# Performance work log

Measured on AMD Instinct MI355X. Metric: run time of the kernel, lower is better.

Reference implementation:

```python
import jax, jax.numpy as jnp
import numpy as np

N, E = 50000, 800000
HID, HEADS, EDIM = 64, 4, 32
HC = HID * HEADS
NEG_SLOPE = 0.2
LN_EPS = 1e-5


def setup_inputs() -> dict:
    key = jax.random.key(0)
    ks = jax.random.split(key, 16)
    s = lambda d: 1.0 / np.sqrt(d)
    return {
        "x": jax.random.normal(ks[0], (N, HID), jnp.float32),
        "edge_index": jax.random.randint(ks[1], (2, E), 0, N, jnp.int64),
        "edge_attr": jax.random.normal(ks[2], (E, EDIM), jnp.float32),
        # GATv2Conv params
        "W_l": jax.random.normal(ks[3], (HID, HC), jnp.float32) * s(HID),
        "b_l": jnp.zeros((HC,), jnp.float32),
        "W_r": jax.random.normal(ks[4], (HID, HC), jnp.float32) * s(HID),
        "b_r": jnp.zeros((HC,), jnp.float32),
        "W_e": jax.random.normal(ks[5], (EDIM, HC), jnp.float32) * s(EDIM),
        "att": jax.random.normal(ks[6], (HEADS, HID), jnp.float32) * s(HID),
        "bias_gat": jnp.zeros((HC,), jnp.float32),
        # block params
        "W1": jax.random.normal(ks[7], (HID, HC), jnp.float32) * s(HID),
        "b1": jnp.zeros((HC,), jnp.float32),
        "gamma": jnp.ones((HC,), jnp.float32),
        "beta": jnp.zeros((HC,), jnp.float32),
        "W2": jax.random.normal(ks[8], (HC, HID), jnp.float32) * s(HC),
        "b2": jnp.zeros((HID,), jnp.float32),
    }


def _gatv2(x, edge_index, edge_attr, W_l, b_l, W_r, b_r, W_e, att, bias_gat):
    src, dst = edge_index[0], edge_index[1]
    x_l = (x @ W_l + b_l).reshape(N, HEADS, HID)  # source transform
    x_r = (x @ W_r + b_r).reshape(N, HEADS, HID)  # target transform
    e = (edge_attr @ W_e).reshape(E, HEADS, HID)
    m = x_l[src] + x_r[dst] + e                    # [E, H, C]
    m = jax.nn.leaky_relu(m, NEG_SLOPE)
    alpha = jnp.einsum('ehc,hc->eh', m, att)       # [E, H]
    # segment softmax over incoming edges of each target node
    amax = jax.ops.segment_max(alpha, dst, num_segments=N)
    alpha = jnp.exp(alpha - amax[dst])
    denom = jax.ops.segment_sum(alpha, dst, num_segments=N)
    alpha = alpha / (denom[dst] + 1e-16)
    out = jax.ops.segment_sum(x_l[src] * alpha[..., None], dst, num_segments=N)
    return out.reshape(N, HC) + bias_gat


def reference(x, edge_index, edge_attr, W_l, b_l, W_r, b_r, W_e, att, bias_gat,
              W1, b1, gamma, beta, W2, b2):
    h = _gatv2(x, edge_index, edge_attr, W_l, b_l, W_r, b_r, W_e, att, bias_gat)
    xl = jnp.tanh(x @ W1 + b1)
    z = xl + h
    mu = jnp.mean(z, axis=-1, keepdims=True)
    var = jnp.var(z, axis=-1, keepdims=True)
    z = (z - mu) * jax.lax.rsqrt(var + LN_EPS) * gamma + beta
    return jnp.tanh(z @ W2 + b2)
```

## Files before the change

kernel.cpp:

```cpp
#include <hip/hip_runtime.h>
#include <math.h>

#define N_NODES 50000
#define N_EDGES 800000
#define HID 64
#define HEADS 4
#define HC 256
#define NEG_SLOPE 0.2f
#define LN_EPS 1e-5f
#define EDGE_BLOCKS 2048

typedef __attribute__((ext_vector_type(8))) short bf16x8;
typedef __attribute__((ext_vector_type(8))) unsigned short u16x8;
typedef __attribute__((ext_vector_type(4))) float f32x4;

__device__ __forceinline__ float bf2f(unsigned short u) {
    return __uint_as_float(((unsigned int)u) << 16);
}
__device__ __forceinline__ unsigned short f2bf(float f) {
    unsigned int u = __float_as_uint(f);
    u = (u + 0x7fffu + ((u >> 16) & 1u)) >> 16;
    return (unsigned short)u;
}
__device__ __forceinline__ float fast_tanh(float v) {
    const float c = fminf(fmaxf(v, -15.f), 15.f);
    const float e = __expf(2.f * c);
    return 1.f - 2.f / (e + 1.f);
}

__global__ __launch_bounds__(256) void k_node_transform(
    const float* __restrict__ x,
    const float* __restrict__ W_l, const float* __restrict__ b_l,
    const float* __restrict__ W_r, const float* __restrict__ b_r,
    unsigned short* __restrict__ xl_t, unsigned short* __restrict__ xr_t)
{
    __shared__ float xs[16][64];
    __shared__ unsigned short tl[16][256], tr[16][256];
    const int n0 = blockIdx.x * 16;
    const int t = threadIdx.x;
    for (int i = t; i < 16 * 64; i += 256) xs[i >> 6][i & 63] = x[n0 * 64 + i];
    __syncthreads();

    float accl[16], accr[16];
    const float bl = b_l[t], br = b_r[t];
#pragma unroll
    for (int n = 0; n < 16; n++) { accl[n] = bl; accr[n] = br; }
    for (int k = 0; k < 64; k++) {
        const float wl = W_l[k * 256 + t];
        const float wr = W_r[k * 256 + t];
#pragma unroll
        for (int n = 0; n < 16; n++) {
            accl[n] = fmaf(xs[n][k], wl, accl[n]);
            accr[n] = fmaf(xs[n][k], wr, accr[n]);
        }
    }
    const int pos = (t & 15) * 16 + (t >> 4);
#pragma unroll
    for (int n = 0; n < 16; n++) {
        tl[n][pos] = f2bf(accl[n]);
        tr[n][pos] = f2bf(accr[n]);
    }
    __syncthreads();
    const int n = t >> 4, q = t & 15;
#pragma unroll
    for (int i = 0; i < 4; i++) {
        *(ushort4*)(xl_t + (size_t)(n0 + n) * 256 + q * 16 + i * 4) = *(const ushort4*)&tl[n][q * 16 + i * 4];
        *(ushort4*)(xr_t + (size_t)(n0 + n) * 256 + q * 16 + i * 4) = *(const ushort4*)&tr[n][q * 16 + i * 4];
    }
}

__global__ __launch_bounds__(256) void k_prep(
    const float* __restrict__ W_e, const float* __restrict__ att,
    unsigned short* __restrict__ wfrag, unsigned short* __restrict__ att_t)
{
    const int t = threadIdx.x;
#pragma unroll
    for (int s = 0; s < 4; s++) {
        const int slot = t * 4 + s;
        const int nt = slot >> 6, ls = slot & 63;
        const int col = nt * 16 + (ls & 15);
        const int kb = (ls >> 4) * 8;
#pragma unroll
        for (int j = 0; j < 8; j++)
            wfrag[slot * 8 + j] = f2bf(W_e[(kb + j) * 256 + col]);
    }
    att_t[t] = f2bf(att[(t & 15) * 16 + (t >> 4)]);
}

__global__ __launch_bounds__(256) void k_hist(const int* __restrict__ ei, int* __restrict__ count)
{
    const int e = blockIdx.x * 256 + threadIdx.x;
    if (e < N_EDGES) atomicAdd(&count[ei[N_EDGES + e]], 1);
}

__global__ __launch_bounds__(1024) void k_scan(const int* __restrict__ count, int* __restrict__ off)
{
    __shared__ int wsum[16];
    __shared__ int s_carry;
    const int t = threadIdx.x, lane = t & 63, wv = t >> 6;
    if (t == 0) s_carry = 0;
    __syncthreads();
    for (int base = 0; base < N_NODES; base += 8192) {
        const int idx0 = base + t * 8;
        int v[8];
#pragma unroll
        for (int j = 0; j < 8; j++) { int i = idx0 + j; v[j] = (i < N_NODES) ? count[i] : 0; }
#pragma unroll
        for (int j = 1; j < 8; j++) v[j] += v[j - 1];
        const int tot = v[7];
        int sc = tot;
#pragma unroll
        for (int s = 1; s < 64; s <<= 1) { int o = __shfl_up(sc, s, 64); if (lane >= s) sc += o; }
        if (lane == 63) wsum[wv] = sc;
        __syncthreads();
        const int carry = s_carry;
        int woff = 0;
        for (int u = 0; u < wv; u++) woff += wsum[u];
        const int ebase = carry + woff + (sc - tot);
#pragma unroll
        for (int j = 0; j < 8; j++) {
            int i = idx0 + j;
            if (i < N_NODES) off[i] = ebase + (j ? v[j - 1] : 0);
        }
        __syncthreads();
        if (t == 0) { int tt = 0; for (int u = 0; u < 16; u++) tt += wsum[u]; s_carry = carry + tt; }
        __syncthreads();
    }
    if (threadIdx.x == 0) off[N_NODES] = s_carry;
}

__global__ __launch_bounds__(256) void k_scatter(
    const int* __restrict__ ei, const int* __restrict__ off, int* __restrict__ cursor,
    const float* __restrict__ edge_attr,
    int* __restrict__ csr_src, unsigned short* __restrict__ ea_csr)
{
    const int e = blockIdx.x * 256 + threadIdx.x;
    if (e < N_EDGES) {
        const int s = ei[e];
        const int d = ei[N_EDGES + e];
        const int pos = off[d] + atomicAdd(&cursor[d], 1);
        csr_src[pos] = s;
        const float4* src4 = (const float4*)(edge_attr + (size_t)e * 32);
        ushort4* dst4 = (ushort4*)(ea_csr + (size_t)pos * 32);
#pragma unroll
        for (int i = 0; i < 8; i++) {
            const float4 v = src4[i];
            ushort4 u;
            u.x = f2bf(v.x); u.y = f2bf(v.y); u.z = f2bf(v.z); u.w = f2bf(v.w);
            dst4[i] = u;
        }
    }
}

template<bool F32>
__global__ __launch_bounds__(256) void k_edgeagg(
    const int* __restrict__ off, const int* __restrict__ csr_src,
    const unsigned short* __restrict__ ea_csr,
    const unsigned short* __restrict__ wfrag, const unsigned short* __restrict__ att_t,
    const unsigned short* __restrict__ xl_t, const unsigned short* __restrict__ xr_t,
    void* __restrict__ zs_g)
{
    __shared__ unsigned short bfrag_s[16][64][8];

    const int t = threadIdx.x;
    const int lane = t & 63, wv = t >> 6;
    const int arow = lane & 15, koct = lane >> 4;

    for (int i = t; i < 1024; i += 256)
        *(u16x8*)&bfrag_s[i >> 6][i & 63][0] = *(const u16x8*)(wfrag + i * 8);
    __syncthreads();

    const u16x8 attL = *(const u16x8*)(att_t + arow * 16);
    const u16x8 attH = *(const u16x8*)(att_t + arow * 16 + 8);

    const int STRIDE = EDGE_BLOCKS * 4;
    int node = blockIdx.x * 4 + wv;
    if (node >= N_NODES) return;

    int lo = off[node], hi = off[node + 1];
    u16x8 xrl = *(const u16x8*)(xr_t + (size_t)node * 256 + arow * 16);
    u16x8 xrh = *(const u16x8*)(xr_t + (size_t)node * 256 + arow * 16 + 8);
    while (hi <= lo) {
#pragma unroll
        for (int q = 0; q < 4; q++) {
            const int nt = koct * 4 + q;
            if (F32) ((float*)zs_g)[(size_t)node * 256 + nt * 16 + arow] = 0.f;
            else ((unsigned short*)zs_g)[(size_t)node * 256 + nt * 16 + arow] = 0;
        }
        node += STRIDE;
        if (node >= N_NODES) return;
        lo = off[node]; hi = off[node + 1];
        xrl = *(const u16x8*)(xr_t + (size_t)node * 256 + arow * 16);
        xrh = *(const u16x8*)(xr_t + (size_t)node * 256 + arow * 16 + 8);
    }
    int svbase = lo;
    int svall = csr_src[min(svbase + lane, hi - 1)];

    int nnode = node + STRIDE;
    bool nvalid = nnode < N_NODES;
    int nlo = 0, nhi = 0, nsvall = 0;
    u16x8 nxrl = xrl, nxrh = xrh;
    if (nvalid) {
        nlo = off[nnode]; nhi = off[nnode + 1];
        nxrl = *(const u16x8*)(xr_t + (size_t)nnode * 256 + arow * 16);
        nxrh = *(const u16x8*)(xr_t + (size_t)nnode * 256 + arow * 16 + 8);
        if (nhi > nlo) nsvall = csr_src[min(nlo + lane, nhi - 1)];
    }
    int p0 = lo;
    bf16x8 af;
    u16x8 xlo[4], xhi[4];
    {
        af = *(const bf16x8*)(ea_csr + (size_t)min(p0 + arow, hi - 1) * 32 + koct * 8);
#pragma unroll
        for (int r = 0; r < 4; r++) {
            const int sr = __shfl(svall, koct * 4 + r, 64);
            const unsigned short* bp = xl_t + (size_t)sr * 256 + arow * 16;
            xlo[r] = *(const u16x8*)bp;
            xhi[r] = *(const u16x8*)(bp + 8);
        }
    }

    float g[16];
#pragma unroll
    for (int i = 0; i < 16; i++) g[i] = 0.f;
    float dsum[4] = {0.f, 0.f, 0.f, 0.f};

    for (;;) {
        const bool last = (p0 + 16 >= hi);
        bool uvalid;
        int up0, uhic;
        if (!last) { uvalid = true; up0 = p0 + 16; uhic = hi; }
        else {
            while (nvalid && nlo >= nhi) {
#pragma unroll
                for (int q = 0; q < 4; q++) {
                    const int nt = koct * 4 + q;
                    if (F32) ((float*)zs_g)[(size_t)nnode * 256 + nt * 16 + arow] = 0.f;
                    else ((unsigned short*)zs_g)[(size_t)nnode * 256 + nt * 16 + arow] = 0;
                }
                nnode += STRIDE;
                nvalid = nnode < N_NODES;
                if (nvalid) {
                    nlo = off[nnode]; nhi = off[nnode + 1];
                    nxrl = *(const u16x8*)(xr_t + (size_t)nnode * 256 + arow * 16);
                    nxrh = *(const u16x8*)(xr_t + (size_t)nnode * 256 + arow * 16 + 8);
                    if (nhi > nlo) nsvall = csr_src[min(nlo + lane, nhi - 1)];
                }
            }
            uvalid = nvalid; up0 = nlo; uhic = nhi;
        }
        bf16x8 uaf = af;
        if (uvalid)
            uaf = *(const bf16x8*)(ea_csr + (size_t)min(up0 + arow, uhic - 1) * 32 + koct * 8);

        float s_[4][4];
#pragma unroll
        for (int r = 0; r < 4; r++)
#pragma unroll
            for (int h = 0; h < 4; h++) s_[r][h] = 0.f;

#pragma unroll
        for (int nt = 0; nt < 8; nt++) {
            const bf16x8 bfr = *(const bf16x8*)&bfrag_s[nt][lane][0];
            const float xrv = bf2f((unsigned short)xrl[nt]);
            f32x4 dacc = {xrv, xrv, xrv, xrv};
            dacc = __builtin_amdgcn_mfma_f32_16x16x32_bf16(af, bfr, dacc, 0, 0, 0);
            const float atv = bf2f((unsigned short)attL[nt]);
            const int h = nt >> 2;
#pragma unroll
            for (int r = 0; r < 4; r++) {
                const float mm = dacc[r] + bf2f((unsigned short)xlo[r][nt]);
                const float lk = fmaxf(mm, NEG_SLOPE * mm);
                s_[r][h] = fmaf(atv, lk, s_[r][h]);
            }
        }
        u16x8 uxlo[4], uxhi[4];
        if (uvalid) {
            const int ubase = last ? 0 : (up0 - svbase);
            const int usrcv = last ? nsvall : svall;
#pragma unroll
            for (int r = 0; r < 4; r++) {
                const int sr = __shfl(usrcv, ubase + koct * 4 + r, 64);
                const unsigned short* bp = xl_t + (size_t)sr * 256 + arow * 16;
                uxlo[r] = *(const u16x8*)bp;
                uxhi[r] = *(const u16x8*)(bp + 8);
            }
        } else {
#pragma unroll
            for (int r = 0; r < 4; r++) { uxlo[r] = xlo[r]; uxhi[r] = xhi[r]; }
        }
#pragma unroll
        for (int n2 = 0; n2 < 8; n2++) {
            const int nt = n2 + 8;
            const bf16x8 bfr = *(const bf16x8*)&bfrag_s[nt][lane][0];
            const float xrv = bf2f((unsigned short)xrh[n2]);
            f32x4 dacc = {xrv, xrv, xrv, xrv};
            dacc = __builtin_amdgcn_mfma_f32_16x16x32_bf16(af, bfr, dacc, 0, 0, 0);
            const float atv = bf2f((unsigned short)attH[n2]);
            const int h = nt >> 2;
#pragma unroll
            for (int r = 0; r < 4; r++) {
                const float mm = dacc[r] + bf2f((unsigned short)xhi[r][n2]);
                const float lk = fmaxf(mm, NEG_SLOPE * mm);
                s_[r][h] = fmaf(atv, lk, s_[r][h]);
            }
        }
#pragma unroll
        for (int r = 0; r < 4; r++)
#pragma unroll
            for (int h = 0; h < 4; h++) {
                float v = s_[r][h];
                v += __shfl_xor(v, 1, 64);
                v += __shfl_xor(v, 2, 64);
                v += __shfl_xor(v, 4, 64);
                v += __shfl_xor(v, 8, 64);
                s_[r][h] = v;
            }
#pragma unroll
        for (int h = 0; h < 4; h++) {
            float w4[4];
#pragma unroll
            for (int r = 0; r < 4; r++) {
                const bool ok = (p0 + koct * 4 + r) < hi;
                w4[r] = ok ? __expf(fminf(s_[r][h], 60.f)) : 0.f;
            }
            dsum[h] += (w4[0] + w4[1]) + (w4[2] + w4[3]);
#pragma unroll
            for (int q = 0; q < 4; q++) {
                const int nt = h * 4 + q;
                float acc = g[nt];
#pragma unroll
                for (int r = 0; r < 4; r++) {
                    const float xv = bf2f((unsigned short)(nt < 8 ? xlo[r][nt & 7] : xhi[r][nt & 7]));
                    acc = fmaf(w4[r], xv, acc);
                }
                g[nt] = acc;
            }
        }

        if (last) {
#pragma unroll
            for (int i = 0; i < 16; i++) {
                float v = g[i];
                v += __shfl_xor(v, 16, 64);
                v += __shfl_xor(v, 32, 64);
                g[i] = v;
            }
#pragma unroll
            for (int h = 0; h < 4; h++) {
                float v = dsum[h];
                v += __shfl_xor(v, 16, 64);
                v += __shfl_xor(v, 32, 64);
                dsum[h] = v;
            }
            float inv[4];
#pragma unroll
            for (int h = 0; h < 4; h++) inv[h] = 1.f / (dsum[h] + 1e-16f);
#pragma unroll
            for (int q = 0; q < 4; q++) {
                const int nt = koct * 4 + q;
                const float v = g[nt] * inv[nt >> 2];
                if (F32) ((float*)zs_g)[(size_t)node * 256 + nt * 16 + arow] = v;
                else ((unsigned short*)zs_g)[(size_t)node * 256 + nt * 16 + arow] = f2bf(v);
            }
            if (!uvalid) return;
            node = nnode; lo = nlo; hi = nhi; xrl = nxrl; xrh = nxrh;
            svbase = nlo; svall = nsvall;
#pragma unroll
            for (int i = 0; i < 16; i++) g[i] = 0.f;
#pragma unroll
            for (int h = 0; h < 4; h++) dsum[h] = 0.f;
            nnode += STRIDE;
            nvalid = nnode < N_NODES;
            if (nvalid) {
                nlo = off[nnode]; nhi = off[nnode + 1];
                nxrl = *(const u16x8*)(xr_t + (size_t)nnode * 256 + arow * 16);
                nxrh = *(const u16x8*)(xr_t + (size_t)nnode * 256 + arow * 16 + 8);
                if (nhi > nlo) nsvall = csr_src[min(nlo + lane, nhi - 1)];
            }
        }
        p0 = up0;
        af = uaf;
#pragma unroll
        for (int r = 0; r < 4; r++) { xlo[r] = uxlo[r]; xhi[r] = uxhi[r]; }
        if (p0 - svbase >= 32) {
            svbase = p0;
            svall = csr_src[min(svbase + lane, hi - 1)];
        }
    }
}

template<bool F32>
__global__ __launch_bounds__(256) void k_post(
    const void* __restrict__ zs_g, const float* __restrict__ x,
    const float* __restrict__ bias_gat,
    const float* __restrict__ W1, const float* __restrict__ b1,
    const float* __restrict__ gamma, const float* __restrict__ beta,
    const float* __restrict__ W2, const float* __restrict__ b2,
    float* __restrict__ out)
{
    __shared__ float xs[16][64];
    __shared__ float zsh[16][256];
    __shared__ float part[16][4][64];
    __shared__ float redS[16][4], redQ[16][4];

    const int n0 = blockIdx.x * 16;
    const int t = threadIdx.x, lane = t & 63, wv = t >> 6;

    for (int i = t; i < 16 * 64; i += 256) xs[i >> 6][i & 63] = x[n0 * 64 + i];
    __syncthreads();

    float a1[16];
    const float b1v = b1[t];
#pragma unroll
    for (int n = 0; n < 16; n++) a1[n] = b1v;
    for (int k = 0; k < 64; k++) {
        const float w1v = W1[k * 256 + t];
#pragma unroll
        for (int n = 0; n < 16; n++) a1[n] = fmaf(xs[n][k], w1v, a1[n]);
    }

    const float bg = bias_gat[t];
    float z[16];
#pragma unroll
    for (int n = 0; n < 16; n++) {
        const float gv = F32 ? ((const float*)zs_g)[(size_t)(n0 + n) * 256 + t]
                             : bf2f(((const unsigned short*)zs_g)[(size_t)(n0 + n) * 256 + t]);
        z[n] = fast_tanh(a1[n]) + gv + bg;
    }

    const float gm = gamma[t], bt = beta[t];
#pragma unroll
    for (int n = 0; n < 16; n++) {
        float s = z[n], q = z[n] * z[n];
#pragma unroll
        for (int m = 1; m < 64; m <<= 1) { s += __shfl_xor(s, m, 64); q += __shfl_xor(q, m, 64); }
        if (lane == 0) { redS[n][wv] = s; redQ[n][wv] = q; }
    }
    __syncthreads();
#pragma unroll
    for (int n = 0; n < 16; n++) {
        const float s = redS[n][0] + redS[n][1] + redS[n][2] + redS[n][3];
        const float q = redQ[n][0] + redQ[n][1] + redQ[n][2] + redQ[n][3];
        const float mu = s * (1.f / 256.f);
        const float var = q * (1.f / 256.f) - mu * mu;
        const float ivn = rsqrtf(var + LN_EPS);
        zsh[n][t] = (z[n] - mu) * ivn * gm + bt;
    }
    __syncthreads();

    const int j = t & 63, qq = t >> 6;
    float p[16];
#pragma unroll
    for (int n = 0; n < 16; n++) p[n] = 0.f;
    for (int c0 = 0; c0 < 64; c0++) {
        const int c = qq * 64 + c0;
        const float w2v = W2[c * 64 + j];
#pragma unroll
        for (int n = 0; n < 16; n++) p[n] = fmaf(zsh[n][c], w2v, p[n]);
    }
#pragma unroll
    for (int n = 0; n < 16; n++) part[n][qq][j] = p[n];
    __syncthreads();
#pragma unroll
    for (int i = 0; i < 4; i++) {
        const int n = wv * 4 + i;
        const float s = part[n][0][lane] + part[n][1][lane] + part[n][2][lane] + part[n][3][lane];
        out[(size_t)(n0 + n) * 64 + lane] = fast_tanh(s + b2[lane]);
    }
}

extern "C" void kernel_launch(void* const* d_in, const int* in_sizes, int n_in,
                              void* d_out, int out_size, void* d_ws, size_t ws_size,
                              hipStream_t stream)
{
    const float* x         = (const float*)d_in[0];
    const int*   ei        = (const int*)d_in[1];
    const float* edge_attr = (const float*)d_in[2];
    const float* W_l       = (const float*)d_in[3];
    const float* b_l       = (const float*)d_in[4];
    const float* W_r       = (const float*)d_in[5];
    const float* b_r       = (const float*)d_in[6];
    const float* W_e       = (const float*)d_in[7];
    const float* att       = (const float*)d_in[8];
    const float* bias_gat  = (const float*)d_in[9];
    const float* W1        = (const float*)d_in[10];
    const float* b1        = (const float*)d_in[11];
    const float* gamma     = (const float*)d_in[12];
    const float* beta      = (const float*)d_in[13];
    const float* W2        = (const float*)d_in[14];
    const float* b2        = (const float*)d_in[15];
    float* out = (float*)d_out;

    char* wsb = (char*)d_ws;
    size_t o = 0;
    unsigned short* xl_t   = (unsigned short*)(wsb + o);  o += (size_t)N_NODES * HC * 2;
    unsigned short* xr_t   = (unsigned short*)(wsb + o);  o += (size_t)N_NODES * HC * 2;
    unsigned short* ea_csr = (unsigned short*)(wsb + o);  o += (size_t)N_EDGES * 32 * 2;
    int* csr_src           = (int*)(wsb + o);             o += (size_t)N_EDGES * 4;
    int* count             = (int*)(wsb + o);             o += (size_t)N_NODES * 4;
    int* cursor            = (int*)(wsb + o);             o += (size_t)N_NODES * 4;
    int* off               = (int*)(wsb + o);             o += (size_t)(N_NODES + 1) * 4;
    unsigned short* wfrag  = (unsigned short*)(wsb + o);  o += 16 * 64 * 8 * 2;
    unsigned short* att_t  = (unsigned short*)(wsb + o);  o += 256 * 2;
    o = (o + 255) & ~(size_t)255;
    void* zs_g             = (void*)(wsb + o);
    const bool f32ok = (o + (size_t)N_NODES * HC * 4) <= ws_size;

    hipMemsetAsync(count, 0, 2 * (size_t)N_NODES * sizeof(int), stream);

    k_node_transform<<<N_NODES / 16, 256, 0, stream>>>(x, W_l, b_l, W_r, b_r, xl_t, xr_t);
    k_prep<<<1, 256, 0, stream>>>(W_e, att, wfrag, att_t);
    k_hist<<<(N_EDGES + 255) / 256, 256, 0, stream>>>(ei, count);
    k_scan<<<1, 1024, 0, stream>>>(count, off);
    k_scatter<<<(N_EDGES + 255) / 256, 256, 0, stream>>>(ei, off, cursor, edge_attr,
                                                         csr_src, ea_csr);
    if (f32ok) {
        k_edgeagg<true><<<EDGE_BLOCKS, 256, 0, stream>>>(off, csr_src, ea_csr, wfrag, att_t,
                                                         xl_t, xr_t, zs_g);
        k_post<true><<<N_NODES / 16, 256, 0, stream>>>(zs_g, x, bias_gat,
                                                       W1, b1, gamma, beta, W2, b2, out);
    } else {
        k_edgeagg<false><<<EDGE_BLOCKS, 256, 0, stream>>>(off, csr_src, ea_csr, wfrag, att_t,
                                                          xl_t, xr_t, zs_g);
        k_post<false><<<N_NODES / 16, 256, 0, stream>>>(zs_g, x, bias_gat,
                                                        W1, b1, gamma, beta, W2, b2, out);
    }
}
```

Baseline: 598.1 us.

## Gather edge attributes by edge id in aggregation instead of permuting them in scatter

```diff
diff --git a/kernel.cpp b/kernel.cpp
--- a/kernel.cpp
+++ b/kernel.cpp
@@ -27,6 +27,12 @@
     const float e = __expf(2.f * c);
     return 1.f - 2.f / (e + 1.f);
 }
+__device__ __forceinline__ bf16x8 pack_bf8(float4 a, float4 b) {
+    u16x8 r;
+    r[0] = f2bf(a.x); r[1] = f2bf(a.y); r[2] = f2bf(a.z); r[3] = f2bf(a.w);
+    r[4] = f2bf(b.x); r[5] = f2bf(b.y); r[6] = f2bf(b.z); r[7] = f2bf(b.w);
+    return __builtin_bit_cast(bf16x8, r);
+}
 
 __global__ __launch_bounds__(256) void k_node_transform(
     const float* __restrict__ x,
@@ -67,24 +73,6 @@
         *(ushort4*)(xl_t + (size_t)(n0 + n) * 256 + q * 16 + i * 4) = *(const ushort4*)&tl[n][q * 16 + i * 4];
         *(ushort4*)(xr_t + (size_t)(n0 + n) * 256 + q * 16 + i * 4) = *(const ushort4*)&tr[n][q * 16 + i * 4];
     }
-}
-
-__global__ __launch_bounds__(256) void k_prep(
-    const float* __restrict__ W_e, const float* __restrict__ att,
-    unsigned short* __restrict__ wfrag, unsigned short* __restrict__ att_t)
-{
-    const int t = threadIdx.x;
-#pragma unroll
-    for (int s = 0; s < 4; s++) {
-        const int slot = t * 4 + s;
-        const int nt = slot >> 6, ls = slot & 63;
-        const int col = nt * 16 + (ls & 15);
-        const int kb = (ls >> 4) * 8;
-#pragma unroll
-        for (int j = 0; j < 8; j++)
-            wfrag[slot * 8 + j] = f2bf(W_e[(kb + j) * 256 + col]);
-    }
-    att_t[t] = f2bf(att[(t & 15) * 16 + (t >> 4)]);
 }
 
 __global__ __launch_bounds__(256) void k_hist(const int* __restrict__ ei, int* __restrict__ count)
@@ -131,8 +119,7 @@
 
 __global__ __launch_bounds__(256) void k_scatter(
     const int* __restrict__ ei, const int* __restrict__ off, int* __restrict__ cursor,
-    const float* __restrict__ edge_attr,
-    int* __restrict__ csr_src, unsigned short* __restrict__ ea_csr)
+    int* __restrict__ csr_src, int* __restrict__ eid_csr)
 {
     const int e = blockIdx.x * 256 + threadIdx.x;
     if (e < N_EDGES) {
@@ -140,23 +127,15 @@
         const int d = ei[N_EDGES + e];
         const int pos = off[d] + atomicAdd(&cursor[d], 1);
         csr_src[pos] = s;
-        const float4* src4 = (const float4*)(edge_attr + (size_t)e * 32);
-        ushort4* dst4 = (ushort4*)(ea_csr + (size_t)pos * 32);
-#pragma unroll
-        for (int i = 0; i < 8; i++) {
-            const float4 v = src4[i];
-            ushort4 u;
-            u.x = f2bf(v.x); u.y = f2bf(v.y); u.z = f2bf(v.z); u.w = f2bf(v.w);
-            dst4[i] = u;
-        }
+        eid_csr[pos] = e;
     }
 }
 
 template<bool F32>
 __global__ __launch_bounds__(256) void k_edgeagg(
     const int* __restrict__ off, const int* __restrict__ csr_src,
-    const unsigned short* __restrict__ ea_csr,
-    const unsigned short* __restrict__ wfrag, const unsigned short* __restrict__ att_t,
+    const int* __restrict__ eid_csr, const float* __restrict__ edge_attr,
+    const float* __restrict__ W_e, const float* __restrict__ att,
     const unsigned short* __restrict__ xl_t, const unsigned short* __restrict__ xr_t,
     void* __restrict__ zs_g)
 {
@@ -166,12 +145,24 @@
     const int lane = t & 63, wv = t >> 6;
     const int arow = lane & 15, koct = lane >> 4;
 
-    for (int i = t; i < 1024; i += 256)
-        *(u16x8*)&bfrag_s[i >> 6][i & 63][0] = *(const u16x8*)(wfrag + i * 8);
-    __syncthreads();
-
-    const u16x8 attL = *(const u16x8*)(att_t + arow * 16);
-    const u16x8 attH = *(const u16x8*)(att_t + arow * 16 + 8);
+    for (int i = t; i < 1024; i += 256) {
+        const int nt = i >> 6, ls = i & 63;
+        const int col = nt * 16 + (ls & 15);
+        const int kb = (ls >> 4) * 8;
+        unsigned short tmp[8];
+#pragma unroll
+        for (int j = 0; j < 8; j++) tmp[j] = f2bf(W_e[(kb + j) * 256 + col]);
+        *(ushort4*)&bfrag_s[nt][ls][0] = make_ushort4(tmp[0], tmp[1], tmp[2], tmp[3]);
+        *(ushort4*)&bfrag_s[nt][ls][4] = make_ushort4(tmp[4], tmp[5], tmp[6], tmp[7]);
+    }
+    __syncthreads();
+
+    float attLf[8], attHf[8];
+#pragma unroll
+    for (int j = 0; j < 8; j++) {
+        attLf[j] = att[j * 16 + arow];
+        attHf[j] = att[(j + 8) * 16 + arow];
+    }
 
     const int STRIDE = EDGE_BLOCKS * 4;
     int node = blockIdx.x * 4 + wv;
@@ -195,22 +186,28 @@
     }
     int svbase = lo;
     int svall = csr_src[min(svbase + lane, hi - 1)];
+    int evall = eid_csr[min(svbase + lane, hi - 1)];
 
     int nnode = node + STRIDE;
     bool nvalid = nnode < N_NODES;
-    int nlo = 0, nhi = 0, nsvall = 0;
+    int nlo = 0, nhi = 0, nsvall = 0, nevall = 0;
     u16x8 nxrl = xrl, nxrh = xrh;
     if (nvalid) {
         nlo = off[nnode]; nhi = off[nnode + 1];
         nxrl = *(const u16x8*)(xr_t + (size_t)nnode * 256 + arow * 16);
         nxrh = *(const u16x8*)(xr_t + (size_t)nnode * 256 + arow * 16 + 8);
-        if (nhi > nlo) nsvall = csr_src[min(nlo + lane, nhi - 1)];
+        if (nhi > nlo) {
+            nsvall = csr_src[min(nlo + lane, nhi - 1)];
+            nevall = eid_csr[min(nlo + lane, nhi - 1)];
+        }
     }
     int p0 = lo;
     bf16x8 af;
     u16x8 xlo[4], xhi[4];
     {
-        af = *(const bf16x8*)(ea_csr + (size_t)min(p0 + arow, hi - 1) * 32 + koct * 8);
+        const int eid0 = __shfl(evall, arow, 64);
+        const float* ap = edge_attr + (size_t)eid0 * 32 + koct * 8;
+        af = pack_bf8(*(const float4*)ap, *(const float4*)(ap + 4));
 #pragma unroll
         for (int r = 0; r < 4; r++) {
             const int sr = __shfl(svall, koct * 4 + r, 64);
@@ -228,8 +225,8 @@
     for (;;) {
         const bool last = (p0 + 16 >= hi);
         bool uvalid;
-        int up0, uhic;
-        if (!last) { uvalid = true; up0 = p0 + 16; uhic = hi; }
+        int up0;
+        if (!last) { uvalid = true; up0 = p0 + 16; }
         else {
             while (nvalid && nlo >= nhi) {
 #pragma unroll
@@ -244,14 +241,23 @@
                     nlo = off[nnode]; nhi = off[nnode + 1];
                     nxrl = *(const u16x8*)(xr_t + (size_t)nnode * 256 + arow * 16);
                     nxrh = *(const u16x8*)(xr_t + (size_t)nnode * 256 + arow * 16 + 8);
-                    if (nhi > nlo) nsvall = csr_src[min(nlo + lane, nhi - 1)];
+                    if (nhi > nlo) {
+                        nsvall = csr_src[min(nlo + lane, nhi - 1)];
+                        nevall = eid_csr[min(nlo + lane, nhi - 1)];
+                    }
                 }
             }
-            uvalid = nvalid; up0 = nlo; uhic = nhi;
-        }
-        bf16x8 uaf = af;
-        if (uvalid)
-            uaf = *(const bf16x8*)(ea_csr + (size_t)min(up0 + arow, uhic - 1) * 32 + koct * 8);
+            uvalid = nvalid; up0 = nlo;
+        }
+        float4 uA0 = make_float4(0.f, 0.f, 0.f, 0.f), uA1 = uA0;
+        if (uvalid) {
+            const int ubase = last ? 0 : (up0 - svbase);
+            const int uev = last ? nevall : evall;
+            const int ueid = __shfl(uev, ubase + arow, 64);
+            const float* ap = edge_attr + (size_t)ueid * 32 + koct * 8;
+            uA0 = *(const float4*)ap;
+            uA1 = *(const float4*)(ap + 4);
+        }
 
         float s_[4][4];
 #pragma unroll
@@ -265,7 +271,7 @@
             const float xrv = bf2f((unsigned short)xrl[nt]);
             f32x4 dacc = {xrv, xrv, xrv, xrv};
             dacc = __builtin_amdgcn_mfma_f32_16x16x32_bf16(af, bfr, dacc, 0, 0, 0);
-            const float atv = bf2f((unsigned short)attL[nt]);
+            const float atv = attLf[nt];
             const int h = nt >> 2;
 #pragma unroll
             for (int r = 0; r < 4; r++) {
@@ -296,7 +302,7 @@
             const float xrv = bf2f((unsigned short)xrh[n2]);
             f32x4 dacc = {xrv, xrv, xrv, xrv};
             dacc = __builtin_amdgcn_mfma_f32_16x16x32_bf16(af, bfr, dacc, 0, 0, 0);
-            const float atv = bf2f((unsigned short)attH[n2]);
+            const float atv = attHf[n2];
             const int h = nt >> 2;
 #pragma unroll
             for (int r = 0; r < 4; r++) {
@@ -365,7 +371,7 @@
             }
             if (!uvalid) return;
             node = nnode; lo = nlo; hi = nhi; xrl = nxrl; xrh = nxrh;
-            svbase = nlo; svall = nsvall;
+            svbase = nlo; svall = nsvall; evall = nevall;
 #pragma unroll
             for (int i = 0; i < 16; i++) g[i] = 0.f;
 #pragma unroll
@@ -376,16 +382,20 @@
                 nlo = off[nnode]; nhi = off[nnode + 1];
                 nxrl = *(const u16x8*)(xr_t + (size_t)nnode * 256 + arow * 16);
                 nxrh = *(const u16x8*)(xr_t + (size_t)nnode * 256 + arow * 16 + 8);
-                if (nhi > nlo) nsvall = csr_src[min(nlo + lane, nhi - 1)];
+                if (nhi > nlo) {
+                    nsvall = csr_src[min(nlo + lane, nhi - 1)];
+                    nevall = eid_csr[min(nlo + lane, nhi - 1)];
+                }
             }
         }
         p0 = up0;
-        af = uaf;
+        af = pack_bf8(uA0, uA1);
 #pragma unroll
         for (int r = 0; r < 4; r++) { xlo[r] = uxlo[r]; xhi[r] = uxhi[r]; }
         if (p0 - svbase >= 32) {
             svbase = p0;
             svall = csr_src[min(svbase + lane, hi - 1)];
+            evall = eid_csr[min(svbase + lane, hi - 1)];
         }
     }
 }
@@ -496,13 +506,11 @@
     size_t o = 0;
     unsigned short* xl_t   = (unsigned short*)(wsb + o);  o += (size_t)N_NODES * HC * 2;
     unsigned short* xr_t   = (unsigned short*)(wsb + o);  o += (size_t)N_NODES * HC * 2;
-    unsigned short* ea_csr = (unsigned short*)(wsb + o);  o += (size_t)N_EDGES * 32 * 2;
     int* csr_src           = (int*)(wsb + o);             o += (size_t)N_EDGES * 4;
+    int* eid_csr           = (int*)(wsb + o);             o += (size_t)N_EDGES * 4;
     int* count             = (int*)(wsb + o);             o += (size_t)N_NODES * 4;
     int* cursor            = (int*)(wsb + o);             o += (size_t)N_NODES * 4;
     int* off               = (int*)(wsb + o);             o += (size_t)(N_NODES + 1) * 4;
-    unsigned short* wfrag  = (unsigned short*)(wsb + o);  o += 16 * 64 * 8 * 2;
-    unsigned short* att_t  = (unsigned short*)(wsb + o);  o += 256 * 2;
     o = (o + 255) & ~(size_t)255;
     void* zs_g             = (void*)(wsb + o);
     const bool f32ok = (o + (size_t)N_NODES * HC * 4) <= ws_size;
@@ -510,19 +518,17 @@
     hipMemsetAsync(count, 0, 2 * (size_t)N_NODES * sizeof(int), stream);
 
     k_node_transform<<<N_NODES / 16, 256, 0, stream>>>(x, W_l, b_l, W_r, b_r, xl_t, xr_t);
-    k_prep<<<1, 256, 0, stream>>>(W_e, att, wfrag, att_t);
     k_hist<<<(N_EDGES + 255) / 256, 256, 0, stream>>>(ei, count);
     k_scan<<<1, 1024, 0, stream>>>(count, off);
-    k_scatter<<<(N_EDGES + 255) / 256, 256, 0, stream>>>(ei, off, cursor, edge_attr,
-                                                         csr_src, ea_csr);
+    k_scatter<<<(N_EDGES + 255) / 256, 256, 0, stream>>>(ei, off, cursor, csr_src, eid_csr);
     if (f32ok) {
-        k_edgeagg<true><<<EDGE_BLOCKS, 256, 0, stream>>>(off, csr_src, ea_csr, wfrag, att_t,
-                                                         xl_t, xr_t, zs_g);
+        k_edgeagg<true><<<EDGE_BLOCKS, 256, 0, stream>>>(off, csr_src, eid_csr, edge_attr,
+                                                         W_e, att, xl_t, xr_t, zs_g);
         k_post<true><<<N_NODES / 16, 256, 0, stream>>>(zs_g, x, bias_gat,
                                                        W1, b1, gamma, beta, W2, b2, out);
     } else {
-        k_edgeagg<false><<<EDGE_BLOCKS, 256, 0, stream>>>(off, csr_src, ea_csr, wfrag, att_t,
-                                                          xl_t, xr_t, zs_g);
+        k_edgeagg<false><<<EDGE_BLOCKS, 256, 0, stream>>>(off, csr_src, eid_csr, edge_attr,
+                                                          W_e, att, xl_t, xr_t, zs_g);
         k_post<false><<<N_NODES / 16, 256, 0, stream>>>(zs_g, x, bias_gat,
                                                         W1, b1, gamma, beta, W2, b2, out);
     }
```

After: 590.0 us. About the same (-1.4%).
